# Kernel tuning notes

Measured on AMD Instinct MI355X. Metric: run time of the kernel, lower is better.

The kernel has to match this reference:

```python
import jax, jax.numpy as jnp
import numpy as np

EMBED = 256
MAX_NL = 2
NP = 9
NH = 1


def bilinear_sample(img, grid):
    # img: [C, H, W]; grid: [N, 2] (x, y) in [-1, 1]
    # F.grid_sample(mode='bilinear', padding_mode='zeros', align_corners=False)
    C, H, W = img.shape
    x = (grid[:, 0] + 1.0) * (W * 0.5) - 0.5
    y = (grid[:, 1] + 1.0) * (H * 0.5) - 0.5
    x0 = jnp.floor(x)
    y0 = jnp.floor(y)
    wx1 = x - x0
    wy1 = y - y0
    img_f = img.reshape(C, H * W)

    def corner(xi, yi, w):
        valid = (xi >= 0) & (xi <= W - 1) & (yi >= 0) & (yi <= H - 1)
        idx = (jnp.clip(yi, 0, H - 1).astype(jnp.int32) * W
               + jnp.clip(xi, 0, W - 1).astype(jnp.int32))
        return img_f[:, idx] * (w * valid)[None, :]

    return (corner(x0, y0, (1 - wx1) * (1 - wy1))
            + corner(x0 + 1, y0, wx1 * (1 - wy1))
            + corner(x0, y0 + 1, (1 - wx1) * wy1)
            + corner(x0 + 1, y0 + 1, wx1 * wy1))  # [C, N]


def setup_inputs() -> dict:
    k = jax.random.key(0)
    ks = jax.random.split(k, 5)
    nq = 20000
    H = W = 128
    nv = H * W
    nl = 2
    C = EMBED
    query = jax.random.normal(ks[0], (1, nq, C), jnp.float32)
    key = jnp.zeros((1, nq, C), jnp.float32)  # unused by forward
    value = jax.random.normal(ks[1], (nl, nv, C), jnp.float32)
    reference_points = jax.random.uniform(ks[2], (1, nq, nl, 2), jnp.float32)
    spatial_shapes = jnp.array([[H, W], [H, W]], jnp.int32)
    W_off = jax.random.normal(ks[3], (C, MAX_NL * NH * NP * 2), jnp.float32) * 0.02
    b_off = jax.random.normal(ks[4], (MAX_NL * NH * NP * 2,), jnp.float32) * 0.02
    return {"query": query, "key": key, "value": value,
            "reference_points": reference_points, "spatial_shapes": spatial_shapes,
            "W_off": W_off, "b_off": b_off}


def reference(query, key, value, reference_points, spatial_shapes, W_off, b_off):
    nl, nv, C = value.shape
    bs, nq, _ = query.shape
    # sampling offsets: [bs, nq, NH, max_nl, NP, 2], sliced to nl levels
    off = (query @ W_off + b_off).reshape(bs, nq, NH, MAX_NL, NP, 2)[:, :, :, :nl]
    # normalizer stacks (W, H) per level
    norm = jnp.stack([spatial_shapes[:, 1], spatial_shapes[:, 0]], -1).astype(query.dtype)
    loc = reference_points[:, :, None, :, None, :] + off / norm[None, None, None, :, None, :]
    grids = 2.0 * loc - 1.0  # [1, nq, 1, nl, NP, 2]
    sampled = []
    for l in range(nl):
        H = int(spatial_shapes[l, 0]); W = int(spatial_shapes[l, 1])
        img = value[l].T.reshape(C, H, W)
        g = grids[0, :, 0, l, :, :].reshape(nq * NP, 2)
        sampled.append(bilinear_sample(img, g).reshape(C, nq, NP))
    # stack levels then flatten points: [1, nq, nl*NP, C]
    kv = jnp.stack(sampled, axis=-2).reshape(C, nq, nl * NP).transpose(1, 2, 0)[None]
    # note: original multiplies by sqrt(dim) (not divide) -- kept faithful
    attn = jax.nn.softmax(jnp.einsum('bqc,bqpc->bqp', query, kv)
                          * jnp.sqrt(jnp.float32(C)), axis=-1)
    return jnp.einsum('bqp,bqpc->bqc', attn, kv)
```

## Files before the change

### kernel.cpp

```cpp
#include <hip/hip_runtime.h>

#define C_EMB 256
#define NPL   9
#define NLV   2
#define NPTS  (NPL * NLV)
#define NJ    (NPTS * 2)

__global__ void transpose_woff(const float* __restrict__ W_off, float* __restrict__ WT) {
    int j = blockIdx.x;
    int c = threadIdx.x;
    WT[j * C_EMB + c] = W_off[c * NJ + j];
}

__device__ __forceinline__ int imin(int a, int b) { return a < b ? a : b; }
__device__ __forceinline__ int imax(int a, int b) { return a > b ? a : b; }

template<int CTRL, int ROW_MASK>
__device__ __forceinline__ float dpp_add(float x) {
    int t = __builtin_amdgcn_update_dpp(0, __builtin_bit_cast(int, x),
                                        CTRL, ROW_MASK, 0xf, true);
    return x + __builtin_bit_cast(float, t);
}

__device__ __forceinline__ float wave_sum_all(float x) {
    x = dpp_add<0x111, 0xf>(x);
    x = dpp_add<0x112, 0xf>(x);
    x = dpp_add<0x114, 0xf>(x);
    x = dpp_add<0x118, 0xf>(x);
    x = dpp_add<0x142, 0xa>(x);
    x = dpp_add<0x143, 0xc>(x);
    int r = __builtin_amdgcn_readlane(__builtin_bit_cast(int, x), 63);
    return __builtin_bit_cast(float, r);
}

template<bool USE_WT>
__global__ __launch_bounds__(128, 3)
void deform_attn_kernel(const float* __restrict__ query,
                        const float* __restrict__ value,
                        const float* __restrict__ refp,
                        const int*   __restrict__ sshapes,
                        const float* __restrict__ WT,
                        const float* __restrict__ W_off,
                        const float* __restrict__ b_off,
                        float*       __restrict__ out,
                        int nq, int nv) {
    const int lane = threadIdx.x & 63;
    const int widx = threadIdx.x >> 6;
    const int q = blockIdx.x * 2 + widx;
    if (q >= nq) return;

    __shared__ int4   s_idx[2][NPTS];
    __shared__ float4 s_w[2][NPTS];

    const int coff  = lane * 4;
    const unsigned coff4 = (unsigned)lane * 16u;
    const float4 q4 = *reinterpret_cast<const float4*>(query + (size_t)q * C_EMB + coff);

    float ox = 0.f, oy = 0.f;
    const char* wtb = (const char*)WT;
    #pragma unroll
    for (int j = 0; j < NJ; ++j) {
        float s;
        if (USE_WT) {
            float4 w4 = *reinterpret_cast<const float4*>(wtb + ((unsigned)(j * 1024) + coff4));
            s = q4.x * w4.x + q4.y * w4.y + q4.z * w4.z + q4.w * w4.w;
        } else {
            const float* wp = W_off + (size_t)coff * NJ + j;
            s = q4.x * wp[0] + q4.y * wp[NJ] + q4.z * wp[2 * NJ] + q4.w * wp[3 * NJ];
        }
        s = wave_sum_all(s) + b_off[j];
        if (j == 2 * lane)     ox = s;
        if (j == 2 * lane + 1) oy = s;
    }

    if (lane < NPTS) {
        int l = lane / NPL;
        int Hi = sshapes[l * 2 + 0];
        int Wi = sshapes[l * 2 + 1];
        float fw = (float)Wi, fh = (float)Hi;
        float rx = refp[((size_t)q * NLV + l) * 2 + 0];
        float ry = refp[((size_t)q * NLV + l) * 2 + 1];
        float x = rx * fw + ox - 0.5f;
        float y = ry * fh + oy - 0.5f;
        float x0f = floorf(x), y0f = floorf(y);
        int x0 = (int)x0f, y0 = (int)y0f;
        float wx1 = x - x0f, wy1 = y - y0f;
        float wx0 = 1.f - wx1, wy0 = 1.f - wy1;
        bool vx0 = (x0 >= 0) && (x0 <= Wi - 1);
        bool vx1 = (x0 + 1 >= 0) && (x0 + 1 <= Wi - 1);
        bool vy0 = (y0 >= 0) && (y0 <= Hi - 1);
        bool vy1 = (y0 + 1 >= 0) && (y0 + 1 <= Hi - 1);
        int cx0 = imin(imax(x0, 0), Wi - 1);
        int cx1 = imin(imax(x0 + 1, 0), Wi - 1);
        int cy0 = imin(imax(y0, 0), Hi - 1);
        int cy1 = imin(imax(y0 + 1, 0), Hi - 1);
        int base = l * nv;
        int4 id;
        id.x = base + cy0 * Wi + cx0;
        id.y = base + cy0 * Wi + cx1;
        id.z = base + cy1 * Wi + cx0;
        id.w = base + cy1 * Wi + cx1;
        float4 w;
        w.x = wx0 * wy0 * ((vx0 && vy0) ? 1.f : 0.f);
        w.y = wx1 * wy0 * ((vx1 && vy0) ? 1.f : 0.f);
        w.z = wx0 * wy1 * ((vx0 && vy1) ? 1.f : 0.f);
        w.w = wx1 * wy1 * ((vx1 && vy1) ? 1.f : 0.f);
        s_idx[widx][lane] = id;
        s_w[widx][lane]   = w;
    }
    __builtin_amdgcn_wave_barrier();

    const char* vb = (const char*)value;
    float m = -3.0e38f, ssum = 0.f;
    float4 o; o.x = 0.f; o.y = 0.f; o.z = 0.f; o.w = 0.f;
    #pragma unroll
    for (int p = 0; p < NPTS; ++p) {
        int4   id = s_idx[widx][p];
        float4 w  = s_w[widx][p];
        const float4 a = *reinterpret_cast<const float4*>(vb + (((unsigned)id.x << 10) + coff4));
        const float4 b = *reinterpret_cast<const float4*>(vb + (((unsigned)id.y << 10) + coff4));
        const float4 c = *reinterpret_cast<const float4*>(vb + (((unsigned)id.z << 10) + coff4));
        const float4 d = *reinterpret_cast<const float4*>(vb + (((unsigned)id.w << 10) + coff4));
        float4 kvp;
        kvp.x = w.x * a.x + w.y * b.x + w.z * c.x + w.w * d.x;
        kvp.y = w.x * a.y + w.y * b.y + w.z * c.y + w.w * d.y;
        kvp.z = w.x * a.z + w.y * b.z + w.z * c.z + w.w * d.z;
        kvp.w = w.x * a.w + w.y * b.w + w.z * c.w + w.w * d.w;
        float dp = q4.x * kvp.x + q4.y * kvp.y + q4.z * kvp.z + q4.w * kvp.w;
        float lg = wave_sum_all(dp) * 16.0f;
        float mn = fmaxf(m, lg);
        float sc = __expf(m - mn);
        float pv = __expf(lg - mn);
        ssum = ssum * sc + pv;
        o.x = o.x * sc + pv * kvp.x;
        o.y = o.y * sc + pv * kvp.y;
        o.z = o.z * sc + pv * kvp.z;
        o.w = o.w * sc + pv * kvp.w;
        m = mn;
    }
    float inv = 1.0f / ssum;
    o.x *= inv; o.y *= inv; o.z *= inv; o.w *= inv;
    *reinterpret_cast<float4*>(out + (size_t)q * C_EMB + coff) = o;
}

extern "C" void kernel_launch(void* const* d_in, const int* in_sizes, int n_in,
                              void* d_out, int out_size, void* d_ws, size_t ws_size,
                              hipStream_t stream) {
    const float* query = (const float*)d_in[0];
    const float* value = (const float*)d_in[2];
    const float* refp  = (const float*)d_in[3];
    const int*   ss    = (const int*)d_in[4];
    const float* W_off = (const float*)d_in[5];
    const float* b_off = (const float*)d_in[6];
    float* out = (float*)d_out;

    const int nq = in_sizes[0] / C_EMB;
    const int nl = in_sizes[4] / 2;
    const int nv = in_sizes[2] / (nl * C_EMB);

    const int blocks = (nq + 1) / 2;

    const size_t wt_bytes = (size_t)NJ * C_EMB * sizeof(float);
    if (ws_size >= wt_bytes) {
        float* WT = (float*)d_ws;
        transpose_woff<<<NJ, C_EMB, 0, stream>>>(W_off, WT);
        deform_attn_kernel<true><<<blocks, 128, 0, stream>>>(
            query, value, refp, ss, WT, W_off, b_off, out, nq, nv);
    } else {
        deform_attn_kernel<false><<<blocks, 128, 0, stream>>>(
            query, value, refp, ss, nullptr, W_off, b_off, out, nq, nv);
    }
}
```

Before: 90.92 us.

## Process two queries per wavefront with 32-lane halves and swizzle reductions

Each 64-lane wavefront now handles two queries, with each 32-lane half covering 8 channels per lane through two float4 loads. The full-wave DPP+readlane reduction becomes a 32-lane reduction using ds_swizzle, which halves the number of reductions per query and doubles the loads in flight per lane. The bias add moves out of the offset loop, the sqrt(C) scale is folded into q, and the occupancy hint in launch_bounds is dropped. Per-lane register pressure goes up, and out-of-range queries are clamped to the last query and recompute it, writing duplicate results.

Result: slower. 98.29 us (+8.1%).

```diff
diff --git a/kernel.cpp b/kernel.cpp
--- a/kernel.cpp
+++ b/kernel.cpp
@@ -22,19 +22,19 @@
     return x + __builtin_bit_cast(float, t);
 }
 
-__device__ __forceinline__ float wave_sum_all(float x) {
+__device__ __forceinline__ float half_sum_all(float x) {
     x = dpp_add<0x111, 0xf>(x);
     x = dpp_add<0x112, 0xf>(x);
     x = dpp_add<0x114, 0xf>(x);
     x = dpp_add<0x118, 0xf>(x);
-    x = dpp_add<0x142, 0xa>(x);
-    x = dpp_add<0x143, 0xc>(x);
-    int r = __builtin_amdgcn_readlane(__builtin_bit_cast(int, x), 63);
+    int t = __builtin_amdgcn_ds_swizzle(__builtin_bit_cast(int, x), 0x401F);
+    x = x + __builtin_bit_cast(float, t);
+    int r = __builtin_amdgcn_ds_swizzle(__builtin_bit_cast(int, x), 0x01F0);
     return __builtin_bit_cast(float, r);
 }
 
 template<bool USE_WT>
-__global__ __launch_bounds__(128, 3)
+__global__ __launch_bounds__(128)
 void deform_attn_kernel(const float* __restrict__ query,
                         const float* __restrict__ value,
                         const float* __restrict__ refp,
@@ -46,15 +46,18 @@
                         int nq, int nv) {
     const int lane = threadIdx.x & 63;
     const int widx = threadIdx.x >> 6;
-    const int q = blockIdx.x * 2 + widx;
-    if (q >= nq) return;
-
-    __shared__ int4   s_idx[2][NPTS];
-    __shared__ float4 s_w[2][NPTS];
-
-    const int coff  = lane * 4;
-    const unsigned coff4 = (unsigned)lane * 16u;
-    const float4 q4 = *reinterpret_cast<const float4*>(query + (size_t)q * C_EMB + coff);
+    const int half = lane >> 5;
+    const int hl   = lane & 31;
+    int q = blockIdx.x * 4 + widx * 2 + half;
+    if (q >= nq) q = nq - 1;
+
+    __shared__ int4   s_idx[2][2][NPTS];
+    __shared__ float4 s_w[2][2][NPTS];
+
+    const unsigned cb = (unsigned)hl * 32u;
+    const char* qb = (const char*)query + (size_t)q * (C_EMB * 4);
+    float4 qa = *reinterpret_cast<const float4*>(qb + cb);
+    float4 qc = *reinterpret_cast<const float4*>(qb + cb + 16);
 
     float ox = 0.f, oy = 0.f;
     const char* wtb = (const char*)WT;
@@ -62,26 +65,31 @@
     for (int j = 0; j < NJ; ++j) {
         float s;
         if (USE_WT) {
-            float4 w4 = *reinterpret_cast<const float4*>(wtb + ((unsigned)(j * 1024) + coff4));
-            s = q4.x * w4.x + q4.y * w4.y + q4.z * w4.z + q4.w * w4.w;
+            float4 wa = *reinterpret_cast<const float4*>(wtb + (unsigned)(j * 1024) + cb);
+            float4 wc = *reinterpret_cast<const float4*>(wtb + (unsigned)(j * 1024) + cb + 16);
+            s = qa.x * wa.x + qa.y * wa.y + qa.z * wa.z + qa.w * wa.w
+              + qc.x * wc.x + qc.y * wc.y + qc.z * wc.z + qc.w * wc.w;
         } else {
-            const float* wp = W_off + (size_t)coff * NJ + j;
-            s = q4.x * wp[0] + q4.y * wp[NJ] + q4.z * wp[2 * NJ] + q4.w * wp[3 * NJ];
+            const float* wp = W_off + (size_t)(hl * 8) * NJ + j;
+            s = qa.x * wp[0 * NJ] + qa.y * wp[1 * NJ] + qa.z * wp[2 * NJ] + qa.w * wp[3 * NJ]
+              + qc.x * wp[4 * NJ] + qc.y * wp[5 * NJ] + qc.z * wp[6 * NJ] + qc.w * wp[7 * NJ];
         }
-        s = wave_sum_all(s) + b_off[j];
-        if (j == 2 * lane)     ox = s;
-        if (j == 2 * lane + 1) oy = s;
-    }
-
-    if (lane < NPTS) {
-        int l = lane / NPL;
+        s = half_sum_all(s);
+        if (j == 2 * hl)     ox = s;
+        if (j == 2 * hl + 1) oy = s;
+    }
+
+    if (hl < NPTS) {
+        int p = hl;
+        int l = p / NPL;
         int Hi = sshapes[l * 2 + 0];
         int Wi = sshapes[l * 2 + 1];
         float fw = (float)Wi, fh = (float)Hi;
         float rx = refp[((size_t)q * NLV + l) * 2 + 0];
         float ry = refp[((size_t)q * NLV + l) * 2 + 1];
-        float x = rx * fw + ox - 0.5f;
-        float y = ry * fh + oy - 0.5f;
+        float2 b2 = *reinterpret_cast<const float2*>(b_off + 2 * p);
+        float x = rx * fw + ox + b2.x - 0.5f;
+        float y = ry * fh + oy + b2.y - 0.5f;
         float x0f = floorf(x), y0f = floorf(y);
         int x0 = (int)x0f, y0 = (int)y0f;
         float wx1 = x - x0f, wy1 = y - y0f;
@@ -105,42 +113,66 @@
         w.y = wx1 * wy0 * ((vx1 && vy0) ? 1.f : 0.f);
         w.z = wx0 * wy1 * ((vx0 && vy1) ? 1.f : 0.f);
         w.w = wx1 * wy1 * ((vx1 && vy1) ? 1.f : 0.f);
-        s_idx[widx][lane] = id;
-        s_w[widx][lane]   = w;
+        s_idx[widx][half][p] = id;
+        s_w[widx][half][p]   = w;
     }
     __builtin_amdgcn_wave_barrier();
+
+    qa.x *= 16.0f; qa.y *= 16.0f; qa.z *= 16.0f; qa.w *= 16.0f;
+    qc.x *= 16.0f; qc.y *= 16.0f; qc.z *= 16.0f; qc.w *= 16.0f;
 
     const char* vb = (const char*)value;
     float m = -3.0e38f, ssum = 0.f;
-    float4 o; o.x = 0.f; o.y = 0.f; o.z = 0.f; o.w = 0.f;
+    float4 oa; oa.x = 0.f; oa.y = 0.f; oa.z = 0.f; oa.w = 0.f;
+    float4 oc; oc.x = 0.f; oc.y = 0.f; oc.z = 0.f; oc.w = 0.f;
     #pragma unroll
     for (int p = 0; p < NPTS; ++p) {
-        int4   id = s_idx[widx][p];
-        float4 w  = s_w[widx][p];
-        const float4 a = *reinterpret_cast<const float4*>(vb + (((unsigned)id.x << 10) + coff4));
-        const float4 b = *reinterpret_cast<const float4*>(vb + (((unsigned)id.y << 10) + coff4));
-        const float4 c = *reinterpret_cast<const float4*>(vb + (((unsigned)id.z << 10) + coff4));
-        const float4 d = *reinterpret_cast<const float4*>(vb + (((unsigned)id.w << 10) + coff4));
-        float4 kvp;
-        kvp.x = w.x * a.x + w.y * b.x + w.z * c.x + w.w * d.x;
-        kvp.y = w.x * a.y + w.y * b.y + w.z * c.y + w.w * d.y;
-        kvp.z = w.x * a.z + w.y * b.z + w.z * c.z + w.w * d.z;
-        kvp.w = w.x * a.w + w.y * b.w + w.z * c.w + w.w * d.w;
-        float dp = q4.x * kvp.x + q4.y * kvp.y + q4.z * kvp.z + q4.w * kvp.w;
-        float lg = wave_sum_all(dp) * 16.0f;
+        int4   id = s_idx[widx][half][p];
+        float4 w  = s_w[widx][half][p];
+        const char* ra = vb + (((unsigned)id.x << 10) + cb);
+        const char* rb = vb + (((unsigned)id.y << 10) + cb);
+        const char* rc = vb + (((unsigned)id.z << 10) + cb);
+        const char* rd = vb + (((unsigned)id.w << 10) + cb);
+        const float4 a0 = *reinterpret_cast<const float4*>(ra);
+        const float4 a1 = *reinterpret_cast<const float4*>(ra + 16);
+        const float4 b0 = *reinterpret_cast<const float4*>(rb);
+        const float4 b1 = *reinterpret_cast<const float4*>(rb + 16);
+        const float4 c0 = *reinterpret_cast<const float4*>(rc);
+        const float4 c1 = *reinterpret_cast<const float4*>(rc + 16);
+        const float4 d0 = *reinterpret_cast<const float4*>(rd);
+        const float4 d1 = *reinterpret_cast<const float4*>(rd + 16);
+        float4 ka, kc;
+        ka.x = w.x * a0.x + w.y * b0.x + w.z * c0.x + w.w * d0.x;
+        ka.y = w.x * a0.y + w.y * b0.y + w.z * c0.y + w.w * d0.y;
+        ka.z = w.x * a0.z + w.y * b0.z + w.z * c0.z + w.w * d0.z;
+        ka.w = w.x * a0.w + w.y * b0.w + w.z * c0.w + w.w * d0.w;
+        kc.x = w.x * a1.x + w.y * b1.x + w.z * c1.x + w.w * d1.x;
+        kc.y = w.x * a1.y + w.y * b1.y + w.z * c1.y + w.w * d1.y;
+        kc.z = w.x * a1.z + w.y * b1.z + w.z * c1.z + w.w * d1.z;
+        kc.w = w.x * a1.w + w.y * b1.w + w.z * c1.w + w.w * d1.w;
+        float dp = qa.x * ka.x + qa.y * ka.y + qa.z * ka.z + qa.w * ka.w
+                 + qc.x * kc.x + qc.y * kc.y + qc.z * kc.z + qc.w * kc.w;
+        float lg = half_sum_all(dp);
         float mn = fmaxf(m, lg);
         float sc = __expf(m - mn);
         float pv = __expf(lg - mn);
         ssum = ssum * sc + pv;
-        o.x = o.x * sc + pv * kvp.x;
-        o.y = o.y * sc + pv * kvp.y;
-        o.z = o.z * sc + pv * kvp.z;
-        o.w = o.w * sc + pv * kvp.w;
+        oa.x = oa.x * sc + pv * ka.x;
+        oa.y = oa.y * sc + pv * ka.y;
+        oa.z = oa.z * sc + pv * ka.z;
+        oa.w = oa.w * sc + pv * ka.w;
+        oc.x = oc.x * sc + pv * kc.x;
+        oc.y = oc.y * sc + pv * kc.y;
+        oc.z = oc.z * sc + pv * kc.z;
+        oc.w = oc.w * sc + pv * kc.w;
         m = mn;
     }
     float inv = 1.0f / ssum;
-    o.x *= inv; o.y *= inv; o.z *= inv; o.w *= inv;
-    *reinterpret_cast<float4*>(out + (size_t)q * C_EMB + coff) = o;
+    oa.x *= inv; oa.y *= inv; oa.z *= inv; oa.w *= inv;
+    oc.x *= inv; oc.y *= inv; oc.z *= inv; oc.w *= inv;
+    char* ob = (char*)out + (size_t)q * (C_EMB * 4);
+    *reinterpret_cast<float4*>(ob + cb)      = oa;
+    *reinterpret_cast<float4*>(ob + cb + 16) = oc;
 }
 
 extern "C" void kernel_launch(void* const* d_in, const int* in_sizes, int n_in,
@@ -158,7 +190,7 @@
     const int nl = in_sizes[4] / 2;
     const int nv = in_sizes[2] / (nl * C_EMB);
 
-    const int blocks = (nq + 1) / 2;
+    const int blocks = (nq + 3) / 4;
 
     const size_t wt_bytes = (size_t)NJ * C_EMB * sizeof(float);
     if (ws_size >= wt_bytes) {
```

## Prefetch bilinear corner values into LDS with async global_load_lds pipeline

Applied to the files above, without the earlier changes.

Replaces the direct global float4 gathers of the four bilinear corners with asynchronous global-to-LDS loads, prefetching two sampling points ahead into a 4-slot per-wave staging buffer. Explicit vmcnt waits and sched barriers pace the pipeline so each point's corners are ready before they are read back from LDS. The aim is to hide gather latency across points. In exchange it adds 32KB of LDS per block, which may limit occupancy, and the launch-bounds occupancy hint is dropped.

After: 102.7 us. +13.0%, slower.

```diff
diff --git a/kernel.cpp b/kernel.cpp
--- a/kernel.cpp
+++ b/kernel.cpp
@@ -1,4 +1,5 @@
 #include <hip/hip_runtime.h>
+#include <stdint.h>
 
 #define C_EMB 256
 #define NPL   9
@@ -33,8 +34,15 @@
     return __builtin_bit_cast(float, r);
 }
 
+__device__ __forceinline__ void async_ld16(const void* g, void* l) {
+    __builtin_amdgcn_global_load_lds(
+        (const __attribute__((address_space(1))) void*)g,
+        (__attribute__((address_space(3))) void*)l,
+        16, 0, 0);
+}
+
 template<bool USE_WT>
-__global__ __launch_bounds__(128, 3)
+__global__ __launch_bounds__(128)
 void deform_attn_kernel(const float* __restrict__ query,
                         const float* __restrict__ value,
                         const float* __restrict__ refp,
@@ -49,11 +57,12 @@
     const int q = blockIdx.x * 2 + widx;
     if (q >= nq) return;
 
+    __shared__ float  stage[2][4][4][C_EMB];
     __shared__ int4   s_idx[2][NPTS];
     __shared__ float4 s_w[2][NPTS];
 
     const int coff  = lane * 4;
-    const unsigned coff4 = (unsigned)lane * 16u;
+    const unsigned cb = (unsigned)lane * 16u;
     const float4 q4 = *reinterpret_cast<const float4*>(query + (size_t)q * C_EMB + coff);
 
     float ox = 0.f, oy = 0.f;
@@ -62,7 +71,7 @@
     for (int j = 0; j < NJ; ++j) {
         float s;
         if (USE_WT) {
-            float4 w4 = *reinterpret_cast<const float4*>(wtb + ((unsigned)(j * 1024) + coff4));
+            float4 w4 = *reinterpret_cast<const float4*>(wtb + (unsigned)(j * 1024) + cb);
             s = q4.x * w4.x + q4.y * w4.y + q4.z * w4.z + q4.w * w4.w;
         } else {
             const float* wp = W_off + (size_t)coff * NJ + j;
@@ -111,16 +120,45 @@
     __builtin_amdgcn_wave_barrier();
 
     const char* vb = (const char*)value;
+
+    __builtin_amdgcn_sched_barrier(0);
+    {
+        int4 id0 = s_idx[widx][0];
+        async_ld16(vb + (((unsigned)id0.x << 10) + cb), &stage[widx][0][0][0]);
+        async_ld16(vb + (((unsigned)id0.y << 10) + cb), &stage[widx][0][1][0]);
+        async_ld16(vb + (((unsigned)id0.z << 10) + cb), &stage[widx][0][2][0]);
+        async_ld16(vb + (((unsigned)id0.w << 10) + cb), &stage[widx][0][3][0]);
+        int4 id1 = s_idx[widx][1];
+        async_ld16(vb + (((unsigned)id1.x << 10) + cb), &stage[widx][1][0][0]);
+        async_ld16(vb + (((unsigned)id1.y << 10) + cb), &stage[widx][1][1][0]);
+        async_ld16(vb + (((unsigned)id1.z << 10) + cb), &stage[widx][1][2][0]);
+        async_ld16(vb + (((unsigned)id1.w << 10) + cb), &stage[widx][1][3][0]);
+    }
+    __builtin_amdgcn_sched_barrier(0);
+
     float m = -3.0e38f, ssum = 0.f;
     float4 o; o.x = 0.f; o.y = 0.f; o.z = 0.f; o.w = 0.f;
     #pragma unroll
     for (int p = 0; p < NPTS; ++p) {
-        int4   id = s_idx[widx][p];
-        float4 w  = s_w[widx][p];
-        const float4 a = *reinterpret_cast<const float4*>(vb + (((unsigned)id.x << 10) + coff4));
-        const float4 b = *reinterpret_cast<const float4*>(vb + (((unsigned)id.y << 10) + coff4));
-        const float4 c = *reinterpret_cast<const float4*>(vb + (((unsigned)id.z << 10) + coff4));
-        const float4 d = *reinterpret_cast<const float4*>(vb + (((unsigned)id.w << 10) + coff4));
+        if (p + 2 < NPTS) {
+            int nb = (p + 2) & 3;
+            int4 id = s_idx[widx][p + 2];
+            async_ld16(vb + (((unsigned)id.x << 10) + cb), &stage[widx][nb][0][0]);
+            async_ld16(vb + (((unsigned)id.y << 10) + cb), &stage[widx][nb][1][0]);
+            async_ld16(vb + (((unsigned)id.z << 10) + cb), &stage[widx][nb][2][0]);
+            async_ld16(vb + (((unsigned)id.w << 10) + cb), &stage[widx][nb][3][0]);
+        }
+        __builtin_amdgcn_sched_barrier(0);
+        if (p < NPTS - 2)       { asm volatile("s_waitcnt vmcnt(8)" ::: "memory"); }
+        else if (p == NPTS - 2) { asm volatile("s_waitcnt vmcnt(4)" ::: "memory"); }
+        else                    { asm volatile("s_waitcnt vmcnt(0)" ::: "memory"); }
+        __builtin_amdgcn_sched_barrier(0);
+        const int buf = p & 3;
+        float4 w = s_w[widx][p];
+        const float4 a = *reinterpret_cast<const float4*>(&stage[widx][buf][0][coff]);
+        const float4 b = *reinterpret_cast<const float4*>(&stage[widx][buf][1][coff]);
+        const float4 c = *reinterpret_cast<const float4*>(&stage[widx][buf][2][coff]);
+        const float4 d = *reinterpret_cast<const float4*>(&stage[widx][buf][3][coff]);
         float4 kvp;
         kvp.x = w.x * a.x + w.y * b.x + w.z * c.x + w.w * d.x;
         kvp.y = w.x * a.y + w.y * b.y + w.z * c.y + w.w * d.y;
@@ -137,6 +175,7 @@
         o.z = o.z * sc + pv * kvp.z;
         o.w = o.w * sc + pv * kvp.w;
         m = mn;
+        __builtin_amdgcn_sched_barrier(0);
     }
     float inv = 1.0f / ssum;
     o.x *= inv; o.y *= inv; o.z *= inv; o.w *= inv;
```
